# Kernel tuning notes

Hardware: AMD Instinct MI355X
Metric: run time of the kernel (lower is better)

## Reference

```python
import jax, jax.numpy as jnp
import numpy as np

HEADS, DIM = 4, 32
HID = HEADS * DIM
K = 8

def gelu(x):
    return jax.nn.gelu(x, approximate=False)

def seg_softmax(logits, seg, n):
    m = jax.ops.segment_max(logits, seg, num_segments=n)
    e = jnp.exp(logits - m[seg])
    s = jax.ops.segment_sum(e, seg, num_segments=n)
    return e / (s[seg] + 1e-16)

def layer_norm(x, g, b, eps=1e-5):
    mu = x.mean(-1, keepdims=True)
    var = ((x - mu) ** 2).mean(-1, keepdims=True)
    return (x - mu) * jax.lax.rsqrt(var + eps) * g + b

def hgt_layer(xa, xb, edges, Wkqv, bkqv, Wout, bout, skip, arel, mrel, prel):
    # One HGTConv: per-type kqv, per-edge-type DxD relation transforms,
    # global scatter-softmax over destination nodes, per-type output + gated skip.
    Na, Nb = xa.shape[0], xb.shape[0]
    N = Na + Nb
    def kqv(x, W, b):
        o = x @ W + b
        k, q, v = jnp.split(o, 3, -1)
        r = lambda t: t.reshape(-1, HEADS, DIM)
        return r(k), r(q), r(v)
    ka, qa, va = kqv(xa, Wkqv[0], bkqv[0])
    kb, qb, vb = kqv(xb, Wkqv[1], bkqv[1])
    # edge types: a->a, a->b, b->a  (dst offset places dst in global node space)
    specs = [(ka, va, qa, 0), (ka, va, qb, Na), (kb, vb, qa, 0)]
    alphas, msgs, dsts = [], [], []
    inv_sqrt_d = np.float32(1.0 / np.sqrt(DIM))
    for et, ((k_s, v_s, q_d, off), ei) in enumerate(zip(specs, edges)):
        src, dst = ei[0], ei[1]
        kt = jnp.einsum('nhd,hde->nhe', k_s, arel[et])  # per-head relation transform
        vt = jnp.einsum('nhd,hde->nhe', v_s, mrel[et])
        a = (q_d[dst] * kt[src]).sum(-1) * prel[et] * inv_sqrt_d  # [E,H]
        alphas.append(a); msgs.append(vt[src]); dsts.append(dst + off)
    alpha = jnp.concatenate(alphas, 0)
    msg = jnp.concatenate(msgs, 0)
    dst = jnp.concatenate(dsts, 0)
    w = seg_softmax(alpha, dst, N)
    agg = jax.ops.segment_sum(w[..., None] * msg, dst, num_segments=N).reshape(N, HID)
    def finish(o, x, t):
        g = gelu(o) @ Wout[t] + bout[t]
        s = jax.nn.sigmoid(skip[t])
        return s * g + (1.0 - s) * x
    return finish(agg[:Na], xa, 0), finish(agg[Na:], xb, 1)

def _forward(x_a, x_b, Wkqv, bkqv, Wout, bout, skip, arel, mrel, prel, ln_g, ln_b,
             Wgat, att_src, att_dst, bgat, W1, b1, W2, b2, W3, b3,
             ei_aa, ei_ab, ei_ba):
    edges = (ei_aa, ei_ab, ei_ba)
    ha, hb = x_a, x_b
    for L in range(3):
        ha, hb = hgt_layer(ha, hb, edges, Wkqv[L], bkqv[L], Wout[L], bout[L],
                           skip[L], arel[L], mrel[L], prel[L])
        if L == 0:  # norm after conv1 only (dropout is identity at inference)
            ha = layer_norm(ha, ln_g[0], ln_b[0])
            hb = layer_norm(hb, ln_g[1], ln_b[1])
        ha, hb = gelu(ha), gelu(hb)
    # to_homogeneous: concat node types in metadata order, offset edge indices
    Na = ha.shape[0]
    h = jnp.concatenate([ha, hb], 0)
    N = h.shape[0]
    loop = jnp.arange(N, dtype=ei_aa.dtype)
    src = jnp.concatenate([ei_aa[0], ei_ab[0], ei_ba[0] + Na, loop])  # GAT adds self loops
    dst = jnp.concatenate([ei_aa[1], ei_ab[1] + Na, ei_ba[1], loop])
    # SAGPooling scorer: GATConv(hid, 1, heads=1)
    x1 = h @ Wgat  # [N,1]
    e = jax.nn.leaky_relu((x1[src] * att_src + x1[dst] * att_dst).sum(-1), 0.2)
    w = seg_softmax(e, dst, N)
    score = (jax.ops.segment_sum(w[:, None] * x1[src], dst, num_segments=N) + bgat).squeeze(-1)
    vals, perm = jax.lax.top_k(score, K)
    hp = (h[perm] * jnp.tanh(vals)[:, None]).reshape(-1)  # [K*HID]
    v = gelu(hp @ W1 + b1)
    v = gelu(v @ W2 + b2)
    v = gelu(v @ W3 + b3)
    return jnp.nan_to_num(v)

def setup_inputs() -> dict:
    key = jax.random.key(0)
    ks = jax.random.split(key, 16)
    Na = Nb = 20000
    E = 150000
    g = lambda i, shape, s: jax.random.normal(ks[i], shape, jnp.float32) * s
    return {
        "x_a": g(0, (Na, 128), 1.0),
        "x_b": g(1, (Nb, 128), 1.0),
        "ei_aa": jax.random.randint(ks[2], (2, E), 0, Na, jnp.int32),
        "ei_ab": jax.random.randint(ks[3], (2, E), 0, Na, jnp.int32),
        "ei_ba": jax.random.randint(ks[4], (2, E), 0, Na, jnp.int32),
        "Wkqv": g(5, (3, 2, 128, 384), 0.05),
        "bkqv": jnp.zeros((3, 2, 384), jnp.float32),
        "Wout": g(6, (3, 2, 128, 128), 0.05),
        "bout": jnp.zeros((3, 2, 128), jnp.float32),
        "skip": jnp.ones((3, 2), jnp.float32),
        "arel": g(7, (3, 3, HEADS, DIM, DIM), 0.1),
        "mrel": g(8, (3, 3, HEADS, DIM, DIM), 0.1),
        "prel": jnp.ones((3, 3, HEADS), jnp.float32),
        "ln_g": jnp.ones((2, 128), jnp.float32),
        "ln_b": jnp.zeros((2, 128), jnp.float32),
        "Wgat": g(9, (128, 1), 0.1),
        "att_src": g(10, (1,), 1.0),
        "att_dst": g(11, (1,), 1.0),
        "bgat": jnp.zeros((1,), jnp.float32),
        "W1": g(12, (K * HID, 128), 0.03),
        "b1": jnp.zeros((128,), jnp.float32),
        "W2": g(13, (128, 64), 0.1),
        "b2": jnp.zeros((64,), jnp.float32),
        "W3": g(14, (64, 16), 0.1),
        "b3": jnp.zeros((16,), jnp.float32),
    }

def reference(x_a, x_b, ei_aa, ei_ab, ei_ba, Wkqv, bkqv, Wout, bout, skip,
              arel, mrel, prel, ln_g, ln_b, Wgat, att_src, att_dst, bgat,
              W1, b1, W2, b2, W3, b3):
    return _forward(x_a, x_b, Wkqv, bkqv, Wout, bout, skip, arel, mrel, prel,
                    ln_g, ln_b, Wgat, att_src, att_dst, bgat,
                    W1, b1, W2, b2, W3, b3, ei_aa, ei_ab, ei_ba)
```

## Files before the change

kernel.cpp:

```cpp
#include <hip/hip_runtime.h>
#include <math.h>

#define HID 128

__device__ __forceinline__ float gelu_f(float x){
  return 0.5f*x*(1.0f+erff(x*0.70710678118654752440f));
}

__global__ void mkw(const float* __restrict__ Wkqv, const float* __restrict__ bkqv,
                    const float* __restrict__ arel, const float* __restrict__ mrel,
                    const float* __restrict__ prel,
                    float* __restrict__ Wc, float* __restrict__ bc) {
  int L = blockIdx.x >> 10;
  int j = blockIdx.x & 1023;
  int t = threadIdx.x;
  int type = (j < 640) ? 0 : 1;
  int jj = (j < 640) ? j : j - 640;
  const float* W    = Wkqv + ((size_t)L*2 + type)*49152;
  const float* bsrc = bkqv + ((size_t)L*2 + type)*384;
  int stride = type ? 384 : 640;
  float* Wdst = Wc + (size_t)L*(640+384)*128 + (type ? (size_t)640*128 : 0);
  float* bdst = bc + (size_t)L*1024 + (type ? 640 : 0);
  float val, bval;
  if (jj < 128) {
    val  = W[(size_t)t*384 + 128 + jj];
    bval = bsrc[128 + jj];
  } else {
    int u = jj - 128;
    int et = type ? 2 : (u >> 8);
    int r = u & 255;
    int h = r >> 6, wofs = r & 63;
    const float* rel; int coloff; float scl;
    if (wofs < 32) {
      rel = arel + ((size_t)L*3 + et)*4096 + (size_t)h*32*32 + wofs;
      coloff = h*32;
      scl = prel[((size_t)L*3 + et)*4 + h] * 0.17677669529663688f * 1.4426950408889634f;
    } else {
      rel = mrel + ((size_t)L*3 + et)*4096 + (size_t)h*32*32 + (wofs - 32);
      coloff = 256 + h*32;
      scl = 1.0f;
    }
    float a = 0.f, bb = 0.f;
    for (int d = 0; d < 32; d++) {
      float rv = rel[(size_t)d*32];
      a  += W[(size_t)t*384 + coloff + d] * rv;
      bb += bsrc[coloff + d] * rv;
    }
    val = a * scl; bval = bb * scl;
  }
  Wdst[(size_t)t*stride + jj] = val;
  if (t == 0) bdst[jj] = bval;
}

__global__ __launch_bounds__(256, 2)
void gemm_tile(const float* __restrict__ x, const float* __restrict__ Wc,
               const float* __restrict__ bc,
               float* __restrict__ qbuf, float* __restrict__ ktv,
               int nrows, int OUT, int qoff, int slot0, int slot1) {
  __shared__ float xs[32][132];
  __shared__ float ws[32][128];
  int tid = threadIdx.x;
  int r0 = blockIdx.x * 128;
  int ct = blockIdx.y;
  int ty = tid >> 4, tx = tid & 15;
  float acc[8][8] = {};
  for (int kc = 0; kc < 128; kc += 32) {
    __syncthreads();
#pragma unroll
    for (int it = 0; it < 4; it++) {
      int idx = it*256 + tid;
      int r = idx >> 3;
      int k4 = (idx & 7) << 2;
      int row = r0 + r;
      float4 v = (row < nrows) ? *(const float4*)(x + (size_t)row*128 + kc + k4)
                               : make_float4(0.f, 0.f, 0.f, 0.f);
      xs[k4+0][r] = v.x; xs[k4+1][r] = v.y; xs[k4+2][r] = v.z; xs[k4+3][r] = v.w;
    }
#pragma unroll
    for (int it = 0; it < 4; it++) {
      int idx = it*256 + tid;
      int k = idx >> 5;
      int c4 = (idx & 31) << 2;
      *(float4*)&ws[k][c4] = *(const float4*)(Wc + (size_t)(kc + k)*OUT + ct*128 + c4);
    }
    __syncthreads();
#pragma unroll
    for (int k = 0; k < 32; k++) {
      float4 a0 = *(const float4*)&xs[k][ty*4];
      float4 a1 = *(const float4*)&xs[k][64 + ty*4];
      float4 b0 = *(const float4*)&ws[k][tx*4];
      float4 b1 = *(const float4*)&ws[k][64 + tx*4];
      float av[8] = {a0.x,a0.y,a0.z,a0.w,a1.x,a1.y,a1.z,a1.w};
      float bv[8] = {b0.x,b0.y,b0.z,b0.w,b1.x,b1.y,b1.z,b1.w};
#pragma unroll
      for (int i = 0; i < 8; i++)
#pragma unroll
        for (int j = 0; j < 8; j++)
          acc[i][j] += av[i]*bv[j];
    }
  }
  bool isq = (ct == 0);
  int sbase = 0, cofs = 0;
  if (!isq) {
    if (ct <= 2) { sbase = slot0; cofs = (ct-1)*128; }
    else         { sbase = slot1; cofs = (ct-3)*128; }
  }
#pragma unroll
  for (int i = 0; i < 8; i++) {
    int r = (i < 4) ? (ty*4 + i) : (64 + ty*4 + i - 4);
    int row = r0 + r;
    if (row >= nrows) continue;
#pragma unroll
    for (int half = 0; half < 2; half++) {
      int c0 = half*64 + tx*4;
      float4 v;
      v.x = acc[i][half*4+0] + bc[ct*128 + c0 + 0];
      v.y = acc[i][half*4+1] + bc[ct*128 + c0 + 1];
      v.z = acc[i][half*4+2] + bc[ct*128 + c0 + 2];
      v.w = acc[i][half*4+3] + bc[ct*128 + c0 + 3];
      if (isq) *(float4*)(qbuf + (size_t)(qoff + row)*128 + c0) = v;
      else     *(float4*)(ktv + (size_t)(sbase + row)*256 + cofs + c0) = v;
    }
  }
}

__global__ __launch_bounds__(256, 2)
void finish_tile(const float* __restrict__ agg,
                 const float* __restrict__ xa, const float* __restrict__ xb,
                 float* __restrict__ ha, float* __restrict__ hb,
                 const float* __restrict__ WoL, const float* __restrict__ boL,
                 const float* __restrict__ skipL, int do_gelu, int Na, int Nb) {
  __shared__ float xs[32][132];
  __shared__ float ws[32][128];
  int nba = (Na + 127) >> 7;
  const float *xsrc, *Wo, *bo; float* h; float sgraw; int nrows, r0, aggoff;
  if ((int)blockIdx.x < nba) {
    xsrc = xa; h = ha; Wo = WoL; bo = boL; sgraw = skipL[0];
    nrows = Na; r0 = blockIdx.x*128; aggoff = 0;
  } else {
    xsrc = xb; h = hb; Wo = WoL + 16384; bo = boL + 128; sgraw = skipL[1];
    nrows = Nb; r0 = ((int)blockIdx.x - nba)*128; aggoff = Na;
  }
  int tid = threadIdx.x;
  int ty = tid >> 4, tx = tid & 15;
  float acc[8][8] = {};
  for (int kc = 0; kc < 128; kc += 32) {
    __syncthreads();
#pragma unroll
    for (int it = 0; it < 4; it++) {
      int idx = it*256 + tid;
      int r = idx >> 3;
      int k4 = (idx & 7) << 2;
      int row = r0 + r;
      float4 v = (row < nrows)
        ? *(const float4*)(agg + (size_t)(aggoff + row)*128 + kc + k4)
        : make_float4(0.f, 0.f, 0.f, 0.f);
      xs[k4+0][r] = gelu_f(v.x); xs[k4+1][r] = gelu_f(v.y);
      xs[k4+2][r] = gelu_f(v.z); xs[k4+3][r] = gelu_f(v.w);
    }
#pragma unroll
    for (int it = 0; it < 4; it++) {
      int idx = it*256 + tid;
      int k = idx >> 5;
      int c4 = (idx & 31) << 2;
      *(float4*)&ws[k][c4] = *(const float4*)(Wo + (size_t)(kc + k)*128 + c4);
    }
    __syncthreads();
#pragma unroll
    for (int k = 0; k < 32; k++) {
      float4 a0 = *(const float4*)&xs[k][ty*4];
      float4 a1 = *(const float4*)&xs[k][64 + ty*4];
      float4 b0 = *(const float4*)&ws[k][tx*4];
      float4 b1 = *(const float4*)&ws[k][64 + tx*4];
      float av[8] = {a0.x,a0.y,a0.z,a0.w,a1.x,a1.y,a1.z,a1.w};
      float bv[8] = {b0.x,b0.y,b0.z,b0.w,b1.x,b1.y,b1.z,b1.w};
#pragma unroll
      for (int i = 0; i < 8; i++)
#pragma unroll
        for (int j = 0; j < 8; j++)
          acc[i][j] += av[i]*bv[j];
    }
  }
  float sg = 1.f/(1.f + expf(-sgraw));
#pragma unroll
  for (int i = 0; i < 8; i++) {
    int r = (i < 4) ? (ty*4 + i) : (64 + ty*4 + i - 4);
    int row = r0 + r;
    if (row >= nrows) continue;
#pragma unroll
    for (int half = 0; half < 2; half++) {
      int c0 = half*64 + tx*4;
      float4 xv = *(const float4*)(xsrc + (size_t)row*128 + c0);
      float4 v;
      v.x = sg*(acc[i][half*4+0] + bo[c0+0]) + (1.f - sg)*xv.x;
      v.y = sg*(acc[i][half*4+1] + bo[c0+1]) + (1.f - sg)*xv.y;
      v.z = sg*(acc[i][half*4+2] + bo[c0+2]) + (1.f - sg)*xv.z;
      v.w = sg*(acc[i][half*4+3] + bo[c0+3]) + (1.f - sg)*xv.w;
      if (do_gelu) { v.x = gelu_f(v.x); v.y = gelu_f(v.y); v.z = gelu_f(v.z); v.w = gelu_f(v.w); }
      *(float4*)(h + (size_t)row*128 + c0) = v;
    }
  }
}

__global__ void hist_init(int* __restrict__ hist, int N) {
  int i = blockIdx.x*blockDim.x + threadIdx.x;
  if (i < N) hist[i] = 0;
}
__global__ void hist_count_all(const int* __restrict__ aa, const int* __restrict__ ab,
                               const int* __restrict__ ba,
                               int Eaa, int Eab, int Eba, int Na, int* __restrict__ hist) {
  int i = blockIdx.x*blockDim.x + threadIdx.x;
  int tot = Eaa + Eab + Eba;
  if (i >= tot) return;
  int dst;
  if (i < Eaa)            dst = aa[Eaa + i];
  else if (i < Eaa + Eab) dst = ab[Eab + (i - Eaa)] + Na;
  else                    dst = ba[Eba + (i - Eaa - Eab)];
  atomicAdd(hist + dst, 1);
}
__global__ void scan_part(const int* __restrict__ hist, int* __restrict__ bsum, int N) {
  __shared__ int sd[256];
  int t = threadIdx.x;
  int i = blockIdx.x*256 + t;
  sd[t] = (i < N) ? hist[i] : 0;
  __syncthreads();
  for (int o = 128; o; o >>= 1) { if (t < o) sd[t] += sd[t+o]; __syncthreads(); }
  if (t == 0) bsum[blockIdx.x] = sd[0];
}
__global__ void scan_bsum(int* __restrict__ bsum, int nb) {
  __shared__ int sd[1024];
  int t = threadIdx.x;
  sd[t] = (t < nb) ? bsum[t] : 0;
  __syncthreads();
  for (int o = 1; o < 1024; o <<= 1) {
    int v = (t >= o) ? sd[t-o] : 0;
    __syncthreads();
    sd[t] += v;
    __syncthreads();
  }
  if (t < nb) bsum[t] = sd[t];
}
__global__ void scan_fill(const int* __restrict__ hist, const int* __restrict__ bsum,
                          int* __restrict__ roff, int* __restrict__ cursor, int N) {
  __shared__ int sd[256];
  int t = threadIdx.x;
  int i = blockIdx.x*256 + t;
  int v = (i < N) ? hist[i] : 0;
  sd[t] = v;
  __syncthreads();
  for (int o = 1; o < 256; o <<= 1) {
    int u = (t >= o) ? sd[t-o] : 0;
    __syncthreads();
    sd[t] += u;
    __syncthreads();
  }
  int boff = (blockIdx.x == 0) ? 0 : bsum[blockIdx.x - 1];
  if (i < N) {
    int excl = boff + sd[t] - v;
    roff[i] = excl;
    cursor[i] = excl;
    if (i == N - 1) roff[N] = boff + sd[t];
  }
}
__global__ void fill_all(const int* __restrict__ aa, const int* __restrict__ ab,
                         const int* __restrict__ ba,
                         int Eaa, int Eab, int Eba, int Na,
                         int* __restrict__ cursor, int* __restrict__ epack) {
  int i = blockIdx.x*blockDim.x + threadIdx.x;
  int tot = Eaa + Eab + Eba;
  if (i >= tot) return;
  int dst, slot;
  if (i < Eaa)            { dst = aa[Eaa + i];                slot = aa[i]; }
  else if (i < Eaa + Eab) { int j = i - Eaa;       dst = ab[Eab + j] + Na; slot = ab[j] + Na; }
  else                    { int j = i - Eaa - Eab; dst = ba[Eba + j];      slot = ba[j] + 2*Na; }
  int pos = atomicAdd(cursor + dst, 1);
  epack[pos] = slot;
}

__global__ void seg_attn(const float* __restrict__ qbuf,
                         const float* __restrict__ ktv,
                         const int* __restrict__ roff, const int* __restrict__ epack,
                         float* __restrict__ agg, int Na, int N) {
  int wid = (blockIdx.x*blockDim.x + threadIdx.x) >> 6;
  int lane = threadIdx.x & 63;
  if (wid >= N) return;
  int quarter = lane >> 4;
  int u = lane & 15;
  int h = u >> 2;
  int d0 = (u & 3) * 8;
  const float* qp = qbuf + (size_t)wid*128 + h*32 + d0;
  float4 qa = *(const float4*)qp;
  float4 qb = *(const float4*)(qp + 4);
  int beg = roff[wid], end = roff[wid + 1];
  float m = -1e30f, s = 0.f;
  float4 aA = make_float4(0.f,0.f,0.f,0.f), aB = make_float4(0.f,0.f,0.f,0.f);
  int i = beg + quarter;
  float4 ka, kb, va, vb;
  if (i < end) {
    const float* kp = ktv + (size_t)epack[i]*256 + h*64 + d0;
    ka = *(const float4*)kp;      kb = *(const float4*)(kp + 4);
    va = *(const float4*)(kp+32); vb = *(const float4*)(kp + 36);
  }
  for (; i < end; i += 4) {
    float4 cka = ka, ckb = kb, cva = va, cvb = vb;
    int nx = i + 4;
    if (nx < end) {
      const float* kp = ktv + (size_t)epack[nx]*256 + h*64 + d0;
      ka = *(const float4*)kp;      kb = *(const float4*)(kp + 4);
      va = *(const float4*)(kp+32); vb = *(const float4*)(kp + 36);
    }
    float sc = qa.x*cka.x + qa.y*cka.y + qa.z*cka.z + qa.w*cka.w
             + qb.x*ckb.x + qb.y*ckb.y + qb.z*ckb.z + qb.w*ckb.w;
    sc += __shfl_xor(sc, 1, 64);
    sc += __shfl_xor(sc, 2, 64);
    float nm = fmaxf(m, sc);
    float scale = exp2f(m - nm);
    float e = exp2f(sc - nm);
    s = s*scale + e;
    aA.x = aA.x*scale + e*cva.x; aA.y = aA.y*scale + e*cva.y;
    aA.z = aA.z*scale + e*cva.z; aA.w = aA.w*scale + e*cva.w;
    aB.x = aB.x*scale + e*cvb.x; aB.y = aB.y*scale + e*cvb.y;
    aB.z = aB.z*scale + e*cvb.z; aB.w = aB.w*scale + e*cvb.w;
    m = nm;
  }
#pragma unroll
  for (int off = 16; off <= 32; off <<= 1) {
    float mo = __shfl_xor(m, off, 64);
    float so = __shfl_xor(s, off, 64);
    float A0 = __shfl_xor(aA.x, off, 64), A1 = __shfl_xor(aA.y, off, 64);
    float A2 = __shfl_xor(aA.z, off, 64), A3 = __shfl_xor(aA.w, off, 64);
    float B0 = __shfl_xor(aB.x, off, 64), B1 = __shfl_xor(aB.y, off, 64);
    float B2 = __shfl_xor(aB.z, off, 64), B3 = __shfl_xor(aB.w, off, 64);
    float nm = fmaxf(m, mo);
    float c1 = exp2f(m - nm), c2 = exp2f(mo - nm);
    s = s*c1 + so*c2;
    aA.x = aA.x*c1 + A0*c2; aA.y = aA.y*c1 + A1*c2;
    aA.z = aA.z*c1 + A2*c2; aA.w = aA.w*c1 + A3*c2;
    aB.x = aB.x*c1 + B0*c2; aB.y = aB.y*c1 + B1*c2;
    aB.z = aB.z*c1 + B2*c2; aB.w = aB.w*c1 + B3*c2;
    m = nm;
  }
  if (quarter == 0) {
    float inv = 1.f / (s + 1e-16f);
    float4 o1, o2;
    o1.x = aA.x*inv; o1.y = aA.y*inv; o1.z = aA.z*inv; o1.w = aA.w*inv;
    o2.x = aB.x*inv; o2.y = aB.y*inv; o2.z = aB.z*inv; o2.w = aB.w*inv;
    float* op = agg + (size_t)wid*128 + h*32 + d0;
    *(float4*)op = o1;
    *(float4*)(op + 4) = o2;
  }
}

__global__ void ln_gelu2(float* __restrict__ h, const float* __restrict__ g,
                         const float* __restrict__ b, int Na, int N) {
  int idx = blockIdx.x*blockDim.x + threadIdx.x;
  int row = idx >> 6, lane = idx & 63;
  if (row >= N) return;
  int po = (row < Na) ? 0 : 128;
  float x0 = h[(size_t)row*128 + lane];
  float x1 = h[(size_t)row*128 + 64 + lane];
  float sum = x0 + x1;
#pragma unroll
  for (int o = 32; o; o >>= 1) sum += __shfl_xor(sum, o, 64);
  float mu = sum * (1.f/128.f);
  float d0 = x0 - mu, d1 = x1 - mu;
  float vs = d0*d0 + d1*d1;
#pragma unroll
  for (int o = 32; o; o >>= 1) vs += __shfl_xor(vs, o, 64);
  float inv = 1.f / sqrtf(vs*(1.f/128.f) + 1e-5f);
  h[(size_t)row*128 + lane]      = gelu_f(d0*inv*g[po + lane] + b[po + lane]);
  h[(size_t)row*128 + 64 + lane] = gelu_f(d1*inv*g[po + 64 + lane] + b[po + 64 + lane]);
}

__global__ void gat_x1(const float* __restrict__ h, const float* __restrict__ Wg,
                       float* __restrict__ x1, int N) {
  int idx = blockIdx.x*blockDim.x + threadIdx.x;
  int row = idx >> 6, lane = idx & 63;
  if (row >= N) return;
  float a = h[(size_t)row*128 + lane]*Wg[lane] + h[(size_t)row*128 + 64 + lane]*Wg[64 + lane];
#pragma unroll
  for (int o = 32; o; o >>= 1) a += __shfl_xor(a, o, 64);
  if (lane == 0) x1[row] = a;
}

__global__ void gat_all(const float* __restrict__ x1, const int* __restrict__ roff,
                        const int* __restrict__ epack,
                        const float* __restrict__ asrc, const float* __restrict__ adst,
                        int Na, int N, float* __restrict__ score) {
  int n = blockIdx.x*blockDim.x + threadIdx.x;
  if (n >= N) return;
  float xd = x1[n];
  float as_ = asrc[0], ad = adst[0];
  float e0 = xd*as_ + xd*ad;
  e0 = (e0 > 0.f) ? e0 : 0.2f*e0;
  float m = e0, s = 1.f, acc = xd;
  int beg = roff[n], end = roff[n + 1];
  for (int i = beg; i < end; i++) {
    int slot = epack[i];
    int sg = (slot < Na) ? slot : slot - Na;
    float xs = x1[sg];
    float e = xs*as_ + xd*ad;
    e = (e > 0.f) ? e : 0.2f*e;
    float nm = fmaxf(m, e);
    float sc = __expf(m - nm), ee = __expf(e - nm);
    s = s*sc + ee;  acc = acc*sc + ee*xs;  m = nm;
  }
  score[n] = acc / (s + 1e-16f);
}

__global__ void topk_stage1(const float* __restrict__ score, const float* __restrict__ bgat,
                            int N, float* __restrict__ cvals, int* __restrict__ cidx) {
  __shared__ float bv[256];
  __shared__ int   bi[256];
  int t = threadIdx.x;
  int chunk = (N + gridDim.x - 1) / gridDim.x;
  int i = blockIdx.x * chunk + t;
  float bg = bgat[0];
  bool valid = (t < chunk && i < N);
  float myv = valid ? score[i] + bg : -INFINITY;
  int   myi = valid ? i : 0x7FFFFFFF;
  for (int k = 0; k < 8; k++) {
    bv[t] = myv; bi[t] = myi;
    __syncthreads();
    for (int o = 128; o; o >>= 1) {
      if (t < o) {
        if (bv[t+o] > bv[t] || (bv[t+o] == bv[t] && bi[t+o] < bi[t])) { bv[t]=bv[t+o]; bi[t]=bi[t+o]; }
      }
      __syncthreads();
    }
    if (t == 0) { cvals[blockIdx.x*8 + k] = bv[0]; cidx[blockIdx.x*8 + k] = bi[0]; }
    if (myi == bi[0]) myv = -INFINITY;
    __syncthreads();
  }
}

__global__ void topk_stage2(const float* __restrict__ cvals, const int* __restrict__ cidx,
                            int C, float* __restrict__ vals, int* __restrict__ perm) {
  __shared__ float bv[256];
  __shared__ int   bi[256];
  __shared__ int   seli[8];
  int t = threadIdx.x;
  for (int k = 0; k < 8; k++) {
    float best = -INFINITY; int besti = 0x7FFFFFFF;
    for (int i = t; i < C; i += 256) {
      int id = cidx[i];
      bool taken = false;
      for (int j = 0; j < k; j++) if (seli[j] == id) taken = true;
      if (taken) continue;
      float v = cvals[i];
      if (v > best || (v == best && id < besti)) { best = v; besti = id; }
    }
    bv[t] = best; bi[t] = besti;
    __syncthreads();
    for (int o = 128; o; o >>= 1) {
      if (t < o) {
        if (bv[t+o] > bv[t] || (bv[t+o] == bv[t] && bi[t+o] < bi[t])) { bv[t]=bv[t+o]; bi[t]=bi[t+o]; }
      }
      __syncthreads();
    }
    if (t == 0) { seli[k] = bi[0]; vals[k] = bv[0]; perm[k] = bi[0]; }
    __syncthreads();
  }
}

__global__ void mlp_final(const float* __restrict__ h, const float* __restrict__ vals,
                          const int* __restrict__ perm,
                          const float* __restrict__ W1, const float* __restrict__ b1,
                          const float* __restrict__ W2, const float* __restrict__ b2,
                          const float* __restrict__ W3, const float* __restrict__ b3,
                          float* __restrict__ out) {
  __shared__ float hp[1024], v1[128], v2[64];
  int t = threadIdx.x;
  for (int i = t; i < 1024; i += 256) {
    int r = i >> 7, d = i & 127;
    hp[i] = h[(size_t)perm[r]*128 + d] * tanhf(vals[r]);
  }
  __syncthreads();
  if (t < 128) {
    float a = 0.f;
    for (int k = 0; k < 1024; k++) a += hp[k]*W1[(size_t)k*128 + t];
    v1[t] = gelu_f(a + b1[t]);
  }
  __syncthreads();
  if (t < 64) {
    float a = 0.f;
    for (int k = 0; k < 128; k++) a += v1[k]*W2[(size_t)k*64 + t];
    v2[t] = gelu_f(a + b2[t]);
  }
  __syncthreads();
  if (t < 16) {
    float a = 0.f;
    for (int k = 0; k < 64; k++) a += v2[k]*W3[(size_t)k*16 + t];
    float r = gelu_f(a + b3[t]);
    if (isnan(r)) r = 0.f;
    else if (isinf(r)) r = (r > 0.f) ? 3.4028234663852886e38f : -3.4028234663852886e38f;
    out[t] = r;
  }
}

extern "C" void kernel_launch(void* const* d_in, const int* in_sizes, int n_in,
                              void* d_out, int out_size, void* d_ws, size_t ws_size,
                              hipStream_t stream) {
  const float* x_a  = (const float*)d_in[0];
  const float* x_b  = (const float*)d_in[1];
  const int* ei_aa  = (const int*)d_in[2];
  const int* ei_ab  = (const int*)d_in[3];
  const int* ei_ba  = (const int*)d_in[4];
  const float* Wkqv = (const float*)d_in[5];
  const float* bkqv = (const float*)d_in[6];
  const float* Wout = (const float*)d_in[7];
  const float* bout = (const float*)d_in[8];
  const float* skip = (const float*)d_in[9];
  const float* arel = (const float*)d_in[10];
  const float* mrel = (const float*)d_in[11];
  const float* prel = (const float*)d_in[12];
  const float* ln_g = (const float*)d_in[13];
  const float* ln_b = (const float*)d_in[14];
  const float* Wgat = (const float*)d_in[15];
  const float* att_src = (const float*)d_in[16];
  const float* att_dst = (const float*)d_in[17];
  const float* bgat = (const float*)d_in[18];
  const float* W1 = (const float*)d_in[19];
  const float* b1 = (const float*)d_in[20];
  const float* W2 = (const float*)d_in[21];
  const float* b2 = (const float*)d_in[22];
  const float* W3 = (const float*)d_in[23];
  const float* b3 = (const float*)d_in[24];

  int Na = in_sizes[0]/128, Nb = in_sizes[1]/128, N = Na + Nb;
  int Eaa = in_sizes[2]/2, Eab = in_sizes[3]/2, Eba = in_sizes[4]/2;
  int Etot = Eaa + Eab + Eba;

  float* w = (float*)d_ws;
  size_t off = 0;
  auto alloc = [&](size_t n) { float* p = w + off; off += n; return p; };
  float* hbuf  = alloc((size_t)N*128);
  float* qbuf  = alloc((size_t)N*128);
  float* ktvA  = alloc((size_t)(2*Na + Nb)*256);
  float* agg   = alloc((size_t)N*128);
  float* Wc    = alloc((size_t)3*1024*128);
  float* bc    = alloc((size_t)3*1024);
  float* x1buf = alloc((size_t)N);
  float* score = alloc((size_t)N);
  float* valsb = alloc(8);
  int*   permb = (int*)alloc(8);
  float* cvals = alloc(2048);
  int*   cidx  = (int*)alloc(2048);
  int*   hist  = (int*)alloc((size_t)N);
  int*   roff  = (int*)alloc((size_t)N + 1);
  int*   cursor= (int*)alloc((size_t)N);
  int*   bsum  = (int*)alloc(1024);
  int*   epack = (int*)alloc((size_t)Etot);

  float* h_a = hbuf;
  float* h_b = hbuf + (size_t)Na*128;

  mkw<<<dim3(3*1024),dim3(128),0,stream>>>(Wkqv, bkqv, arel, mrel, prel, Wc, bc);

  int nsb = (N + 255)/256;
  hist_init<<<dim3(nsb),dim3(256),0,stream>>>(hist, N);
  hist_count_all<<<dim3((Etot+255)/256),dim3(256),0,stream>>>(ei_aa, ei_ab, ei_ba, Eaa, Eab, Eba, Na, hist);
  scan_part<<<dim3(nsb),dim3(256),0,stream>>>(hist, bsum, N);
  scan_bsum<<<dim3(1),dim3(1024),0,stream>>>(bsum, nsb);
  scan_fill<<<dim3(nsb),dim3(256),0,stream>>>(hist, bsum, roff, cursor, N);
  fill_all<<<dim3((Etot+255)/256),dim3(256),0,stream>>>(ei_aa, ei_ab, ei_ba, Eaa, Eab, Eba, Na, cursor, epack);

  int nba = (Na + 127)/128, nbb = (Nb + 127)/128;

  for (int L = 0; L < 3; L++) {
    const float* xa_in = (L == 0) ? x_a : h_a;
    const float* xb_in = (L == 0) ? x_b : h_b;
    const float* WcA = Wc + (size_t)L*1024*128;
    const float* WcB = WcA + (size_t)640*128;
    const float* bcA = bc + (size_t)L*1024;
    const float* bcB = bcA + 640;
    gemm_tile<<<dim3(nba, 5),dim3(256),0,stream>>>(xa_in, WcA, bcA, qbuf, ktvA, Na, 640, 0,  0,    Na);
    gemm_tile<<<dim3(nbb, 3),dim3(256),0,stream>>>(xb_in, WcB, bcB, qbuf, ktvA, Nb, 384, Na, 2*Na, 2*Na);
    seg_attn<<<dim3((N+3)/4),dim3(256),0,stream>>>(qbuf, ktvA, roff, epack, agg, Na, N);
    int do_gelu = (L == 0) ? 0 : 1;
    finish_tile<<<dim3(nba + nbb),dim3(256),0,stream>>>(agg, xa_in, xb_in, h_a, h_b,
                                                        Wout + (size_t)L*2*16384,
                                                        bout + (size_t)L*2*128,
                                                        skip + L*2, do_gelu, Na, Nb);
    if (L == 0) {
      ln_gelu2<<<dim3((N+3)/4),dim3(256),0,stream>>>(hbuf, ln_g, ln_b, Na, N);
    }
  }

  gat_x1<<<dim3((N+3)/4),dim3(256),0,stream>>>(hbuf, Wgat, x1buf, N);
  gat_all<<<dim3((N+255)/256),dim3(256),0,stream>>>(x1buf, roff, epack, att_src, att_dst, Na, N, score);
  int tk_blocks = (N + 255)/256;
  topk_stage1<<<dim3(tk_blocks),dim3(256),0,stream>>>(score, bgat, N, cvals, cidx);
  topk_stage2<<<dim3(1),dim3(256),0,stream>>>(cvals, cidx, tk_blocks*8, valsb, permb);
  mlp_final<<<dim3(1),dim3(256),0,stream>>>(hbuf, valsb, permb, W1, b1, W2, b2, W3, b3, (float*)d_out);
}
```

Baseline: 822.0 us.

## Fuse LN, GAT projection and top-k/MLP into neighbours; merge kqv GEMMs; deepen prefetch

Merges the two per-type kqv GEMM launches into one flat-grid launch. Folds the layer-0 LayerNorm+GELU and the final GAT x1 projection into the finish_tile epilogue using 16-lane shuffles. Merges top-k stage 2 with the final MLP kernel, and deepens the seg_attn edge prefetch from one to two iterations ahead. The aim is to remove several small launches and extra full passes over the hidden buffer. The cost is more register pressure in finish_tile and seg_attn, plus extra branching in the epilogue.

```diff
diff --git a/kernel.cpp b/kernel.cpp
--- a/kernel.cpp
+++ b/kernel.cpp
@@ -53,15 +53,20 @@
 }
 
 __global__ __launch_bounds__(256, 2)
-void gemm_tile(const float* __restrict__ x, const float* __restrict__ Wc,
-               const float* __restrict__ bc,
-               float* __restrict__ qbuf, float* __restrict__ ktv,
-               int nrows, int OUT, int qoff, int slot0, int slot1) {
+void gemm_tile2(const float* __restrict__ xa, const float* __restrict__ xb,
+                const float* __restrict__ WcA, const float* __restrict__ WcB,
+                const float* __restrict__ bcA, const float* __restrict__ bcB,
+                float* __restrict__ qbuf, float* __restrict__ ktv,
+                int Na, int Nb, int nba, int nbb) {
   __shared__ float xs[32][132];
   __shared__ float ws[32][128];
+  int bid = blockIdx.x;
+  bool typeA = bid < nba*5;
+  const float *x, *Wc, *bc;
+  int nrows, r0, ct, OUT;
+  if (typeA) { ct = bid / nba; int rb = bid % nba; x = xa; Wc = WcA; bc = bcA; nrows = Na; r0 = rb*128; OUT = 640; }
+  else { int idx = bid - nba*5; ct = idx / nbb; int rb = idx % nbb; x = xb; Wc = WcB; bc = bcB; nrows = Nb; r0 = rb*128; OUT = 384; }
   int tid = threadIdx.x;
-  int r0 = blockIdx.x * 128;
-  int ct = blockIdx.y;
   int ty = tid >> 4, tx = tid & 15;
   float acc[8][8] = {};
   for (int kc = 0; kc < 128; kc += 32) {
@@ -100,10 +105,11 @@
     }
   }
   bool isq = (ct == 0);
+  int qoff = typeA ? 0 : Na;
   int sbase = 0, cofs = 0;
   if (!isq) {
-    if (ct <= 2) { sbase = slot0; cofs = (ct-1)*128; }
-    else         { sbase = slot1; cofs = (ct-3)*128; }
+    if (typeA) { if (ct <= 2) { sbase = 0;  cofs = (ct-1)*128; } else { sbase = Na; cofs = (ct-3)*128; } }
+    else       { sbase = 2*Na; cofs = (ct-1)*128; }
   }
 #pragma unroll
   for (int i = 0; i < 8; i++) {
@@ -129,17 +135,20 @@
                  const float* __restrict__ xa, const float* __restrict__ xb,
                  float* __restrict__ ha, float* __restrict__ hb,
                  const float* __restrict__ WoL, const float* __restrict__ boL,
-                 const float* __restrict__ skipL, int do_gelu, int Na, int Nb) {
+                 const float* __restrict__ skipL,
+                 const float* __restrict__ lng, const float* __restrict__ lnb,
+                 const float* __restrict__ Wg, float* __restrict__ x1,
+                 int mode, int Na, int Nb) {
   __shared__ float xs[32][132];
   __shared__ float ws[32][128];
   int nba = (Na + 127) >> 7;
-  const float *xsrc, *Wo, *bo; float* h; float sgraw; int nrows, r0, aggoff;
+  const float *xsrc, *Wo, *bo; float* h; float sgraw; int nrows, r0, aggoff, po;
   if ((int)blockIdx.x < nba) {
     xsrc = xa; h = ha; Wo = WoL; bo = boL; sgraw = skipL[0];
-    nrows = Na; r0 = blockIdx.x*128; aggoff = 0;
+    nrows = Na; r0 = blockIdx.x*128; aggoff = 0; po = 0;
   } else {
     xsrc = xb; h = hb; Wo = WoL + 16384; bo = boL + 128; sgraw = skipL[1];
-    nrows = Nb; r0 = ((int)blockIdx.x - nba)*128; aggoff = Na;
+    nrows = Nb; r0 = ((int)blockIdx.x - nba)*128; aggoff = Na; po = 128;
   }
   int tid = threadIdx.x;
   int ty = tid >> 4, tx = tid & 15;
@@ -187,17 +196,48 @@
     int r = (i < 4) ? (ty*4 + i) : (64 + ty*4 + i - 4);
     int row = r0 + r;
     if (row >= nrows) continue;
-#pragma unroll
-    for (int half = 0; half < 2; half++) {
-      int c0 = half*64 + tx*4;
-      float4 xv = *(const float4*)(xsrc + (size_t)row*128 + c0);
-      float4 v;
-      v.x = sg*(acc[i][half*4+0] + bo[c0+0]) + (1.f - sg)*xv.x;
-      v.y = sg*(acc[i][half*4+1] + bo[c0+1]) + (1.f - sg)*xv.y;
-      v.z = sg*(acc[i][half*4+2] + bo[c0+2]) + (1.f - sg)*xv.z;
-      v.w = sg*(acc[i][half*4+3] + bo[c0+3]) + (1.f - sg)*xv.w;
-      if (do_gelu) { v.x = gelu_f(v.x); v.y = gelu_f(v.y); v.z = gelu_f(v.z); v.w = gelu_f(v.w); }
-      *(float4*)(h + (size_t)row*128 + c0) = v;
+    int c0 = tx*4, c1 = 64 + tx*4;
+    float4 xv0 = *(const float4*)(xsrc + (size_t)row*128 + c0);
+    float4 xv1 = *(const float4*)(xsrc + (size_t)row*128 + c1);
+    float v[8];
+    v[0] = sg*(acc[i][0] + bo[c0+0]) + (1.f-sg)*xv0.x;
+    v[1] = sg*(acc[i][1] + bo[c0+1]) + (1.f-sg)*xv0.y;
+    v[2] = sg*(acc[i][2] + bo[c0+2]) + (1.f-sg)*xv0.z;
+    v[3] = sg*(acc[i][3] + bo[c0+3]) + (1.f-sg)*xv0.w;
+    v[4] = sg*(acc[i][4] + bo[c1+0]) + (1.f-sg)*xv1.x;
+    v[5] = sg*(acc[i][5] + bo[c1+1]) + (1.f-sg)*xv1.y;
+    v[6] = sg*(acc[i][6] + bo[c1+2]) + (1.f-sg)*xv1.z;
+    v[7] = sg*(acc[i][7] + bo[c1+3]) + (1.f-sg)*xv1.w;
+    if (mode == 0) {
+      float sum = v[0]+v[1]+v[2]+v[3]+v[4]+v[5]+v[6]+v[7];
+      sum += __shfl_xor(sum, 1, 64); sum += __shfl_xor(sum, 2, 64);
+      sum += __shfl_xor(sum, 4, 64); sum += __shfl_xor(sum, 8, 64);
+      float mu = sum * (1.f/128.f);
+      float var = 0.f;
+#pragma unroll
+      for (int j = 0; j < 8; j++) { float d = v[j]-mu; var += d*d; }
+      var += __shfl_xor(var, 1, 64); var += __shfl_xor(var, 2, 64);
+      var += __shfl_xor(var, 4, 64); var += __shfl_xor(var, 8, 64);
+      float inv = 1.f / sqrtf(var*(1.f/128.f) + 1e-5f);
+#pragma unroll
+      for (int j = 0; j < 8; j++) {
+        int c = (j < 4) ? (c0 + j) : (c1 + j - 4);
+        v[j] = gelu_f((v[j]-mu)*inv*lng[po + c] + lnb[po + c]);
+      }
+    } else {
+#pragma unroll
+      for (int j = 0; j < 8; j++) v[j] = gelu_f(v[j]);
+    }
+    float4 o0; o0.x=v[0]; o0.y=v[1]; o0.z=v[2]; o0.w=v[3];
+    float4 o1; o1.x=v[4]; o1.y=v[5]; o1.z=v[6]; o1.w=v[7];
+    *(float4*)(h + (size_t)row*128 + c0) = o0;
+    *(float4*)(h + (size_t)row*128 + c1) = o1;
+    if (mode == 2) {
+      float s1 = v[0]*Wg[c0+0] + v[1]*Wg[c0+1] + v[2]*Wg[c0+2] + v[3]*Wg[c0+3]
+               + v[4]*Wg[c1+0] + v[5]*Wg[c1+1] + v[6]*Wg[c1+2] + v[7]*Wg[c1+3];
+      s1 += __shfl_xor(s1, 1, 64); s1 += __shfl_xor(s1, 2, 64);
+      s1 += __shfl_xor(s1, 4, 64); s1 += __shfl_xor(s1, 8, 64);
+      if (tx == 0) x1[(size_t)aggoff ? (size_t)row + Na : (size_t)row] = s1;
     }
   }
 }
@@ -295,19 +335,25 @@
   float m = -1e30f, s = 0.f;
   float4 aA = make_float4(0.f,0.f,0.f,0.f), aB = make_float4(0.f,0.f,0.f,0.f);
   int i = beg + quarter;
-  float4 ka, kb, va, vb;
+  float4 ka0, kb0, va0, vb0, ka1, kb1, va1, vb1;
   if (i < end) {
     const float* kp = ktv + (size_t)epack[i]*256 + h*64 + d0;
-    ka = *(const float4*)kp;      kb = *(const float4*)(kp + 4);
-    va = *(const float4*)(kp+32); vb = *(const float4*)(kp + 36);
+    ka0 = *(const float4*)kp;      kb0 = *(const float4*)(kp + 4);
+    va0 = *(const float4*)(kp+32); vb0 = *(const float4*)(kp + 36);
+  }
+  if (i + 4 < end) {
+    const float* kp = ktv + (size_t)epack[i+4]*256 + h*64 + d0;
+    ka1 = *(const float4*)kp;      kb1 = *(const float4*)(kp + 4);
+    va1 = *(const float4*)(kp+32); vb1 = *(const float4*)(kp + 36);
   }
   for (; i < end; i += 4) {
-    float4 cka = ka, ckb = kb, cva = va, cvb = vb;
-    int nx = i + 4;
+    float4 cka = ka0, ckb = kb0, cva = va0, cvb = vb0;
+    ka0 = ka1; kb0 = kb1; va0 = va1; vb0 = vb1;
+    int nx = i + 8;
     if (nx < end) {
       const float* kp = ktv + (size_t)epack[nx]*256 + h*64 + d0;
-      ka = *(const float4*)kp;      kb = *(const float4*)(kp + 4);
-      va = *(const float4*)(kp+32); vb = *(const float4*)(kp + 36);
+      ka1 = *(const float4*)kp;      kb1 = *(const float4*)(kp + 4);
+      va1 = *(const float4*)(kp+32); vb1 = *(const float4*)(kp + 36);
     }
     float sc = qa.x*cka.x + qa.y*cka.y + qa.z*cka.z + qa.w*cka.w
              + qb.x*ckb.x + qb.y*ckb.y + qb.z*ckb.z + qb.w*ckb.w;
@@ -349,38 +395,6 @@
     *(float4*)op = o1;
     *(float4*)(op + 4) = o2;
   }
-}
-
-__global__ void ln_gelu2(float* __restrict__ h, const float* __restrict__ g,
-                         const float* __restrict__ b, int Na, int N) {
-  int idx = blockIdx.x*blockDim.x + threadIdx.x;
-  int row = idx >> 6, lane = idx & 63;
-  if (row >= N) return;
-  int po = (row < Na) ? 0 : 128;
-  float x0 = h[(size_t)row*128 + lane];
-  float x1 = h[(size_t)row*128 + 64 + lane];
-  float sum = x0 + x1;
-#pragma unroll
-  for (int o = 32; o; o >>= 1) sum += __shfl_xor(sum, o, 64);
-  float mu = sum * (1.f/128.f);
-  float d0 = x0 - mu, d1 = x1 - mu;
-  float vs = d0*d0 + d1*d1;
-#pragma unroll
-  for (int o = 32; o; o >>= 1) vs += __shfl_xor(vs, o, 64);
-  float inv = 1.f / sqrtf(vs*(1.f/128.f) + 1e-5f);
-  h[(size_t)row*128 + lane]      = gelu_f(d0*inv*g[po + lane] + b[po + lane]);
-  h[(size_t)row*128 + 64 + lane] = gelu_f(d1*inv*g[po + 64 + lane] + b[po + 64 + lane]);
-}
-
-__global__ void gat_x1(const float* __restrict__ h, const float* __restrict__ Wg,
-                       float* __restrict__ x1, int N) {
-  int idx = blockIdx.x*blockDim.x + threadIdx.x;
-  int row = idx >> 6, lane = idx & 63;
-  if (row >= N) return;
-  float a = h[(size_t)row*128 + lane]*Wg[lane] + h[(size_t)row*128 + 64 + lane]*Wg[64 + lane];
-#pragma unroll
-  for (int o = 32; o; o >>= 1) a += __shfl_xor(a, o, 64);
-  if (lane == 0) x1[row] = a;
 }
 
 __global__ void gat_all(const float* __restrict__ x1, const int* __restrict__ roff,
@@ -434,11 +448,17 @@
   }
 }
 
-__global__ void topk_stage2(const float* __restrict__ cvals, const int* __restrict__ cidx,
-                            int C, float* __restrict__ vals, int* __restrict__ perm) {
+__global__ void topk_mlp(const float* __restrict__ cvals, const int* __restrict__ cidx, int C,
+                         const float* __restrict__ h,
+                         const float* __restrict__ W1, const float* __restrict__ b1,
+                         const float* __restrict__ W2, const float* __restrict__ b2,
+                         const float* __restrict__ W3, const float* __restrict__ b3,
+                         float* __restrict__ out) {
   __shared__ float bv[256];
   __shared__ int   bi[256];
   __shared__ int   seli[8];
+  __shared__ float sval[8];
+  __shared__ float hp[1024], v1[128], v2[64];
   int t = threadIdx.x;
   for (int k = 0; k < 8; k++) {
     float best = -INFINITY; int besti = 0x7FFFFFFF;
@@ -458,22 +478,12 @@
       }
       __syncthreads();
     }
-    if (t == 0) { seli[k] = bi[0]; vals[k] = bv[0]; perm[k] = bi[0]; }
-    __syncthreads();
-  }
-}
-
-__global__ void mlp_final(const float* __restrict__ h, const float* __restrict__ vals,
-                          const int* __restrict__ perm,
-                          const float* __restrict__ W1, const float* __restrict__ b1,
-                          const float* __restrict__ W2, const float* __restrict__ b2,
-                          const float* __restrict__ W3, const float* __restrict__ b3,
-                          float* __restrict__ out) {
-  __shared__ float hp[1024], v1[128], v2[64];
-  int t = threadIdx.x;
+    if (t == 0) { seli[k] = bi[0]; sval[k] = bv[0]; }
+    __syncthreads();
+  }
   for (int i = t; i < 1024; i += 256) {
     int r = i >> 7, d = i & 127;
-    hp[i] = h[(size_t)perm[r]*128 + d] * tanhf(vals[r]);
+    hp[i] = h[(size_t)seli[r]*128 + d] * tanhf(sval[r]);
   }
   __syncthreads();
   if (t < 128) {
@@ -542,8 +552,6 @@
   float* bc    = alloc((size_t)3*1024);
   float* x1buf = alloc((size_t)N);
   float* score = alloc((size_t)N);
-  float* valsb = alloc(8);
-  int*   permb = (int*)alloc(8);
   float* cvals = alloc(2048);
   int*   cidx  = (int*)alloc(2048);
   int*   hist  = (int*)alloc((size_t)N);
@@ -574,23 +582,20 @@
     const float* WcB = WcA + (size_t)640*128;
     const float* bcA = bc + (size_t)L*1024;
     const float* bcB = bcA + 640;
-    gemm_tile<<<dim3(nba, 5),dim3(256),0,stream>>>(xa_in, WcA, bcA, qbuf, ktvA, Na, 640, 0,  0,    Na);
-    gemm_tile<<<dim3(nbb, 3),dim3(256),0,stream>>>(xb_in, WcB, bcB, qbuf, ktvA, Nb, 384, Na, 2*Na, 2*Na);
+    gemm_tile2<<<dim3(nba*5 + nbb*3),dim3(256),0,stream>>>(xa_in, xb_in, WcA, WcB, bcA, bcB,
+                                                           qbuf, ktvA, Na, Nb, nba, nbb);
     seg_attn<<<dim3((N+3)/4),dim3(256),0,stream>>>(qbuf, ktvA, roff, epack, agg, Na, N);
-    int do_gelu = (L == 0) ? 0 : 1;
+    int mode = (L == 0) ? 0 : (L == 2 ? 2 : 1);
     finish_tile<<<dim3(nba + nbb),dim3(256),0,stream>>>(agg, xa_in, xb_in, h_a, h_b,
                                                         Wout + (size_t)L*2*16384,
                                                         bout + (size_t)L*2*128,
-                                                        skip + L*2, do_gelu, Na, Nb);
-    if (L == 0) {
-      ln_gelu2<<<dim3((N+3)/4),dim3(256),0,stream>>>(hbuf, ln_g, ln_b, Na, N);
-    }
-  }
-
-  gat_x1<<<dim3((N+3)/4),dim3(256),0,stream>>>(hbuf, Wgat, x1buf, N);
+                                                        skip + L*2, ln_g, ln_b,
+                                                        Wgat, x1buf, mode, Na, Nb);
+  }
+
   gat_all<<<dim3((N+255)/256),dim3(256),0,stream>>>(x1buf, roff, epack, att_src, att_dst, Na, N, score);
   int tk_blocks = (N + 255)/256;
   topk_stage1<<<dim3(tk_blocks),dim3(256),0,stream>>>(score, bgat, N, cvals, cidx);
-  topk_stage2<<<dim3(1),dim3(256),0,stream>>>(cvals, cidx, tk_blocks*8, valsb, permb);
-  mlp_final<<<dim3(1),dim3(256),0,stream>>>(hbuf, valsb, permb, W1, b1, W2, b2, W3, b3, (float*)d_out);
-}
+  topk_mlp<<<dim3(1),dim3(256),0,stream>>>(cvals, cidx, tk_blocks*8, hbuf,
+                                           W1, b1, W2, b2, W3, b3, (float*)d_out);
+}
```

New measurement: 781.2 us. 5.0% less time.
